# Kernel tuning notes

Measured on AMD Instinct MI355X. Metric: run time of the kernel, lower is better.

The kernel has to match this reference:

```python
import jax, jax.numpy as jnp
import numpy as np

B, L, DH = 4, 4096, 1024
T, DG = 1024, 768
P = 256


def setup_inputs() -> dict:
    key = jax.random.key(0)
    k1, k2, k3, k4, k5 = jax.random.split(key, 5)
    H = jax.random.normal(k1, (B, L, DH), dtype=jnp.float32)
    G = jax.random.normal(k2, (B, T, DG), dtype=jnp.float32)
    # key mask: True = padded/masked. Guarantee at least one valid key per row.
    mask = jax.random.randint(k3, (B, L), 0, 2).astype(jnp.bool_)
    mask = mask.at[:, 0].set(False)
    # torch Linear weights: [out, in]
    Wk_w = jax.random.normal(k4, (P, DH), dtype=jnp.float32) * (DH ** -0.5)
    Wq_w = jax.random.normal(k5, (P, DG), dtype=jnp.float32) * (DG ** -0.5)
    return {"H": H, "G": G, "mask": mask, "Wk_w": Wk_w, "Wq_w": Wq_w}


def reference(H, G, mask, Wk_w, Wq_w):
    # K = Wk(H): [B,L,P]; Q = Wq(G): [B,T,P]
    K = jnp.einsum('bld,pd->blp', H, Wk_w)
    Q = jnp.einsum('btd,pd->btp', G, Wq_w)
    scale = P ** -0.5
    logits = jnp.einsum('btp,blp->btl', Q, K) * scale  # [B,T,L]
    neg_inf = jnp.finfo(logits.dtype).min
    logits = jnp.where(mask[:, None, :], neg_inf, logits)
    alpha = jax.nn.softmax(logits, axis=-1)  # softmax over L (streaming-equivalent)
    Z = jnp.einsum('btl,bld->btd', alpha, H)  # [B,T,DH]
    return Z
```

## Files before the change

kernel.cpp:

```cpp
#include <hip/hip_runtime.h>
#include <hip/hip_bf16.h>


typedef __attribute__((ext_vector_type(8))) short short8;
typedef __attribute__((ext_vector_type(4))) float f32x4;

static __device__ __forceinline__ unsigned short bf16bits(float x) {
    __hip_bfloat16 b = __float2bfloat16(x);
    return *(unsigned short*)&b;
}

static __device__ __forceinline__ void gload_lds16(const __hip_bfloat16* g,
                                                   __hip_bfloat16* l)
{
    auto gp = (const __attribute__((address_space(1))) unsigned int*)(uintptr_t)g;
    auto lp = (__attribute__((address_space(3))) unsigned int*)(unsigned int)(uintptr_t)l;
    __builtin_amdgcn_global_load_lds(gp, lp, 16, 0, 0);
}

__global__ __launch_bounds__(256)
void scan_kernel(const void* __restrict__ mask,
                 unsigned short* __restrict__ idx,
                 int* __restrict__ lc, int* __restrict__ lcpad,
                 float* __restrict__ rowsum, int L, int T, int B)
{
    const int b = blockIdx.x;
    const int tid = threadIdx.x;

    for (int i = tid; i < T; i += 256) rowsum[(long)b * T + i] = 0.f;

    const unsigned char*  m8g  = (const unsigned char*)mask;
    const unsigned short* m16g = (const unsigned short*)mask;
    const unsigned int*   m32g = (const unsigned int*)mask;
    __shared__ int c1, c2, c4, c8, cp, wsh;
    if (tid == 0) { c1 = c2 = c4 = c8 = cp = 0; }
    __syncthreads();
    {
        const int N = B * L;
        int l1 = 0, l2 = 0, l4 = 0, l8 = 0, lp = 0;
        for (int i = tid; i < N; i += 256) l1 += (m8g[i] != 0);
        for (int i = tid; i < N / 2; i += 256) {
            l2 += (m16g[i] != 0);
            lp += ((m8g[2 * i] != 0) == (m8g[2 * i + 1] != 0));
        }
        for (int i = tid; i < N / 4; i += 256) l4 += (m32g[i] != 0);
        for (int i = tid; i < N / 8; i += 256) l8 += ((m32g[2 * i] | m32g[2 * i + 1]) != 0);
        atomicAdd(&c1, l1); atomicAdd(&c2, l2); atomicAdd(&c4, l4);
        atomicAdd(&c8, l8); atomicAdd(&cp, lp);
    }
    __syncthreads();
    if (tid == 0) {
        const float f1 = fabsf(c1 / 16384.f - 0.5f);
        const float f2 = fabsf(c2 / 8192.f  - 0.5f);
        const float f4 = fabsf(c4 / 4096.f  - 0.5f);
        const float f8 = fabsf(c8 / 2048.f  - 0.5f);
        int w = 1; float best = f1;
        if (f2 < best) { best = f2; w = 2; }
        if (f4 < best) { best = f4; w = 4; }
        if (f8 < best) { best = f8; w = 8; }
        if (w == 1 && cp > 7400) w = 2;
        wsh = w;
    }
    __syncthreads();
    const int w = wsh;

    const unsigned char*  m8  = (const unsigned char*)mask;
    const unsigned short* m16 = (const unsigned short*)mask;
    const unsigned int*   m32 = (const unsigned int*)mask;
    const uint2*          m64 = (const uint2*)mask;
    bool v[16];
    int cnt = 0;
    #pragma unroll
    for (int i = 0; i < 16; ++i) {
        const int l = tid * 16 + i;
        const long mi = (long)b * L + l;
        bool masked;
        if (w == 1)      masked = m8[mi] != 0;
        else if (w == 2) masked = m16[mi] != 0;
        else if (w == 4) masked = m32[mi] != 0;
        else             { uint2 q = m64[mi]; masked = (q.x | q.y) != 0; }
        v[i] = !masked;
        cnt += v[i] ? 1 : 0;
    }
    __shared__ int waveTot[4];
    int pre = cnt;
    #pragma unroll
    for (int off = 1; off < 64; off <<= 1) {
        const int t = __shfl_up(pre, off, 64);
        if ((tid & 63) >= off) pre += t;
    }
    if ((tid & 63) == 63) waveTot[tid >> 6] = pre;
    __syncthreads();
    int waveOff = 0;
    for (int wv = 0; wv < (tid >> 6); ++wv) waveOff += waveTot[wv];
    int o = waveOff + pre - cnt;
    #pragma unroll
    for (int i = 0; i < 16; ++i)
        if (v[i]) idx[(long)b * L + (o++)] = (unsigned short)(tid * 16 + i);
    if (tid == 255) {
        const int total = waveOff + pre;
        lc[b] = total;
        lcpad[b] = (total + 127) & ~127;
    }
}

__global__ __launch_bounds__(256)
void prep_all_kernel(const float* __restrict__ H,
                     __hip_bfloat16* __restrict__ Hbf,
                     __hip_bfloat16* __restrict__ Ht,
                     const unsigned short* __restrict__ idx,
                     const int* __restrict__ lc, const int* __restrict__ lcpad,
                     const float* __restrict__ Wk, unsigned short* __restrict__ Wkbf,
                     const float* __restrict__ Wq, unsigned short* __restrict__ Wqbf,
                     const float* __restrict__ G,  unsigned short* __restrict__ Gbf,
                     int L, int D)
{
    __shared__ __align__(16) __hip_bfloat16 tile[64][72];
    int id = blockIdx.x;
    if (id < 4096) {
        const int b  = id >> 10;
        const int c0 = (id & 63) * 64;
        if (c0 >= lcpad[b]) return;
        const int d0 = ((id >> 6) & 15) * 64;
        const int Lcb = lc[b];
        const float* Hb = H + (long)b * L * D;
        __hip_bfloat16* Hbfb = Hbf + (long)b * L * D;
        __hip_bfloat16* Htb  = Ht  + (long)b * D * L;
        const int tx = threadIdx.x & 15, ty = threadIdx.x >> 4;
        #pragma unroll
        for (int p = 0; p < 4; ++p) {
            const int row = ty + p * 16;
            const int c = c0 + row;
            float4 v = {0.f, 0.f, 0.f, 0.f};
            if (c < Lcb) {
                const int l = idx[(long)b * L + c];
                v = *(const float4*)(&Hb[(long)l * D + d0 + tx * 4]);
            }
            ushort4 o;
            o.x = bf16bits(v.x); o.y = bf16bits(v.y);
            o.z = bf16bits(v.z); o.w = bf16bits(v.w);
            *(ushort4*)(&Hbfb[(long)c * D + d0 + tx * 4]) = o;
            tile[tx * 4 + 0][row] = __float2bfloat16(v.x);
            tile[tx * 4 + 1][row] = __float2bfloat16(v.y);
            tile[tx * 4 + 2][row] = __float2bfloat16(v.z);
            tile[tx * 4 + 3][row] = __float2bfloat16(v.w);
        }
        __syncthreads();
        const int ll = threadIdx.x & 7;
        const int dq = threadIdx.x >> 3;
        #pragma unroll
        for (int q = 0; q < 2; ++q) {
            const int dd = dq + q * 32;
            const short8 v = *(const short8*)(&tile[dd][ll * 8]);
            *(short8*)(&Htb[(long)(d0 + dd) * L + c0 + ll * 8]) = v;
        }
        return;
    }
    id -= 4096;
    const float* in; unsigned short* out; int n4;
    if (id < 256)       { in = Wk; out = Wkbf; n4 = (256 * 1024) / 4; }
    else if (id < 448)  { id -= 256; in = Wq; out = Wqbf; n4 = (256 * 768) / 4; }
    else                { id -= 448; in = G;  out = Gbf;  n4 = (4 * 1024 * 768) / 4; }
    const int i = id * 256 + threadIdx.x;
    if (i >= n4) return;
    float4 v = ((const float4*)in)[i];
    ushort4 o;
    o.x = bf16bits(v.x); o.y = bf16bits(v.y);
    o.z = bf16bits(v.z); o.w = bf16bits(v.w);
    ((ushort4*)out)[i] = o;
}

template <typename OutT, int SPLITK, int MODE, int CMODE>
static __device__ __forceinline__
void gemm_bt_body(int bx, int by, int bz, __hip_bfloat16* lds_pool,
                  const __hip_bfloat16* __restrict__ A,
                  const __hip_bfloat16* __restrict__ Bm,
                  OutT* __restrict__ C,
                  int K, int lda, int ldb, int ldc,
                  long batchStrideA, long batchStrideB, long batchStrideC,
                  float scale,
                  float* __restrict__ rowsum, int rowsumStride,
                  long partStride,
                  const int* __restrict__ lc, const int* __restrict__ lcpad,
                  int Lfull)
{
    const int zb = bz / SPLITK;
    const int kc = bz % SPLITK;
    const int rowBase = bx * 128;
    const int colBase = by * 128;

    if constexpr (CMODE == 1) {
        const int bb = rowBase / Lfull;
        if (rowBase - bb * Lfull >= lcpad[bb]) return;
    }
    if constexpr (CMODE == 2) {
        if (colBase >= lcpad[zb]) return;
    }

    A  += (long)zb * batchStrideA;
    Bm += (long)zb * batchStrideB;
    C  += (long)zb * batchStrideC + (long)kc * partStride;
    int Kdyn = K;
    if constexpr (CMODE == 3) Kdyn = lcpad[zb];
    const int Kloc  = Kdyn / SPLITK;
    const int kbase = kc * Kloc;
    const int NT    = Kloc / 32;

    const int tid  = threadIdx.x;
    const int lane = tid & 63;
    const int wave = tid >> 6;
    const int wm = (wave & 1) * 64;
    const int wn = (wave >> 1) * 64;

    __hip_bfloat16* AsP = lds_pool;
    __hip_bfloat16* BsP = lds_pool + 12288;

    f32x4 acc[4][4];
    #pragma unroll
    for (int i = 0; i < 4; ++i)
        #pragma unroll
        for (int j = 0; j < 4; ++j)
            acc[i][j] = (f32x4){0.f, 0.f, 0.f, 0.f};

    const int srow = lane >> 2;
    const int scol = ((lane & 3) ^ ((lane >> 3) & 3)) * 8;
    const long ar0 = (long)(rowBase + wave * 32 + srow) * lda;
    const long ar1 = ar0 + 16l * lda;
    const long br0 = (long)(colBase + wave * 32 + srow) * ldb;
    const long br1 = br0 + 16l * ldb;

    const int mrow = lane & 15;
    const int koff = (((lane >> 4) ^ ((lane >> 1) & 3)) * 8);

    auto stage = [&](int buf, int t) {
        const int kk = kbase + t * 32 + scol;
        gload_lds16(A  + ar0 + kk, AsP + buf * 4096 + wave * 1024);
        gload_lds16(A  + ar1 + kk, AsP + buf * 4096 + wave * 1024 + 512);
        gload_lds16(Bm + br0 + kk, BsP + buf * 4096 + wave * 1024);
        gload_lds16(Bm + br1 + kk, BsP + buf * 4096 + wave * 1024 + 512);
    };

    stage(0, 0);
    if (NT > 1) stage(1, 1);

    int cur = 0;
    for (int t = 0; t < NT; ++t) {
        if (t + 1 < NT)
            asm volatile("s_waitcnt vmcnt(4)" ::: "memory");
        else
            asm volatile("s_waitcnt vmcnt(0)" ::: "memory");
        __builtin_amdgcn_s_barrier();
        if (t + 2 < NT) {
            const int nxt2 = (cur >= 1) ? cur - 1 : cur + 2;
            stage(nxt2, t + 2);
        }

        short8 af[4], bf[4];
        #pragma unroll
        for (int mi = 0; mi < 4; ++mi)
            af[mi] = *(const short8*)(AsP + cur * 4096 + (wm + mi * 16 + mrow) * 32 + koff);
        #pragma unroll
        for (int ni = 0; ni < 4; ++ni)
            bf[ni] = *(const short8*)(BsP + cur * 4096 + (wn + ni * 16 + mrow) * 32 + koff);

        #pragma unroll
        for (int mi = 0; mi < 4; ++mi)
            #pragma unroll
            for (int ni = 0; ni < 4; ++ni)
                acc[mi][ni] = __builtin_amdgcn_mfma_f32_16x16x32_bf16(
                    af[mi], bf[ni], acc[mi][ni], 0, 0, 0);
        cur = (cur == 2) ? 0 : cur + 1;
    }

    const int crow0 = (lane >> 4) * 4;
    const int ccol  = lane & 15;

    if constexpr (MODE == 2 || sizeof(OutT) == 2) {
        __syncthreads();
        __hip_bfloat16* cst = lds_pool;

        if constexpr (MODE == 2) {
            const int lcv = lc[zb];
            bool mk[4];
            #pragma unroll
            for (int ni = 0; ni < 4; ++ni)
                mk[ni] = (colBase + wn + ni * 16 + ccol) >= lcv;
            #pragma unroll
            for (int mi = 0; mi < 4; ++mi) {
                #pragma unroll
                for (int r = 0; r < 4; ++r) {
                    const int row = wm + mi * 16 + crow0 + r;
                    float rs = 0.f;
                    #pragma unroll
                    for (int ni = 0; ni < 4; ++ni) {
                        const int col = wn + ni * 16 + ccol;
                        const float e = mk[ni] ? 0.f
                                               : __expf(acc[mi][ni][r] * scale);
                        const __hip_bfloat16 pb = __float2bfloat16(e);
                        cst[row * 136 + (((col >> 3) ^ (row >> 3)) << 3) + (col & 7)] = pb;
                        rs += __bfloat162float(pb);
                    }
                    rs += __shfl_xor(rs, 1, 64);
                    rs += __shfl_xor(rs, 2, 64);
                    rs += __shfl_xor(rs, 4, 64);
                    rs += __shfl_xor(rs, 8, 64);
                    if ((lane & 15) == 0)
                        atomicAdd(&rowsum[(long)zb * rowsumStride + rowBase + row], rs);
                }
            }
        } else {
            #pragma unroll
            for (int mi = 0; mi < 4; ++mi) {
                #pragma unroll
                for (int ni = 0; ni < 4; ++ni) {
                    #pragma unroll
                    for (int r = 0; r < 4; ++r) {
                        const int row = wm + mi * 16 + crow0 + r;
                        const int col = wn + ni * 16 + ccol;
                        cst[row * 136 + (((col >> 3) ^ (row >> 3)) << 3) + (col & 7)] =
                            __float2bfloat16(acc[mi][ni][r] * scale);
                    }
                }
            }
        }
        __syncthreads();
        const int g   = tid & 15;
        const int r4  = tid >> 4;
        const int lof = ((g ^ r4) << 3);
        #pragma unroll
        for (int k = 0; k < 8; ++k) {
            const int row = r4 * 8 + k;
            const short8 v = *(const short8*)(cst + row * 136 + lof);
            *(short8*)(&((__hip_bfloat16*)C)[(long)(rowBase + row) * ldc + colBase + g * 8]) = v;
        }
    } else {
        #pragma unroll
        for (int mi = 0; mi < 4; ++mi) {
            #pragma unroll
            for (int ni = 0; ni < 4; ++ni) {
                #pragma unroll
                for (int r = 0; r < 4; ++r) {
                    const int row = rowBase + wm + mi * 16 + crow0 + r;
                    const int col = colBase + wn + ni * 16 + ccol;
                    ((float*)C)[(long)row * ldc + col] = acc[mi][ni][r] * scale;
                }
            }
        }
    }
}

static __device__ __forceinline__ void xcd_swizzle(int& bx, int& by, int& bz)
{
    const int nwg = gridDim.x * gridDim.y * gridDim.z;
    bx = blockIdx.x; by = blockIdx.y; bz = blockIdx.z;
    if ((nwg & 7) == 0) {
        int lin = bx + gridDim.x * (by + gridDim.y * bz);
        lin = (lin & 7) * (nwg >> 3) + (lin >> 3);
        bx = lin % gridDim.x;
        const int t = lin / gridDim.x;
        by = t % gridDim.y;
        bz = t / gridDim.y;
    }
}

template <typename OutT, int SPLITK, int MODE, int CMODE>
__global__ __launch_bounds__(256)
void gemm_bt_kernel(const __hip_bfloat16* __restrict__ A,
                    const __hip_bfloat16* __restrict__ Bm,
                    OutT* __restrict__ C,
                    int K, int lda, int ldb, int ldc,
                    long batchStrideA, long batchStrideB, long batchStrideC,
                    float scale,
                    float* __restrict__ rowsum, int rowsumStride,
                    long partStride,
                    const int* __restrict__ lc, const int* __restrict__ lcpad,
                    int Lfull)
{
    __shared__ __align__(16) __hip_bfloat16 lds_pool[24576];
    int bx, by, bz;
    xcd_swizzle(bx, by, bz);
    gemm_bt_body<OutT, SPLITK, MODE, CMODE>(bx, by, bz, lds_pool,
        A, Bm, C, K, lda, ldb, ldc, batchStrideA, batchStrideB, batchStrideC,
        scale, rowsum, rowsumStride, partStride, lc, lcpad, Lfull);
}

__global__ __launch_bounds__(256)
void qk_gemm_kernel(const __hip_bfloat16* __restrict__ Gbf,
                    const __hip_bfloat16* __restrict__ Wqbf,
                    __hip_bfloat16* __restrict__ Qbf,
                    const __hip_bfloat16* __restrict__ Hbf,
                    const __hip_bfloat16* __restrict__ Wkbf,
                    __hip_bfloat16* __restrict__ Kbf,
                    const int* __restrict__ lcpad,
                    int DG_, int DH_, int P_, int L_)
{
    __shared__ __align__(16) __hip_bfloat16 lds_pool[24576];
    int bx, by, bz;
    xcd_swizzle(bx, by, bz);
    if (bx < 32) {
        gemm_bt_body<__hip_bfloat16, 1, 0, 0>(bx, by, 0, lds_pool,
            Gbf, Wqbf, Qbf, DG_, DG_, DG_, P_, 0, 0, 0, 1.0f,
            nullptr, 0, 0, nullptr, nullptr, 0);
    } else {
        gemm_bt_body<__hip_bfloat16, 1, 0, 1>(bx - 32, by, 0, lds_pool,
            Hbf, Wkbf, Kbf, DH_, DH_, DH_, P_, 0, 0, 0, 1.0f,
            nullptr, 0, 0, nullptr, lcpad, L_);
    }
}

__global__ __launch_bounds__(256)
void combine_kernel(const float* __restrict__ Zp,
                    const float* __restrict__ rowsum,
                    float* __restrict__ Z, long partStride)
{
    const int i = blockIdx.x * 256 + threadIdx.x;
    const float4 a = ((const float4*)Zp)[i];
    const float4 b = ((const float4*)(Zp + partStride))[i];
    const float inv = 1.0f / rowsum[i >> 8];
    float4 o;
    o.x = (a.x + b.x) * inv;
    o.y = (a.y + b.y) * inv;
    o.z = (a.z + b.z) * inv;
    o.w = (a.w + b.w) * inv;
    ((float4*)Z)[i] = o;
}

extern "C" void kernel_launch(void* const* d_in, const int* in_sizes, int n_in,
                              void* d_out, int out_size, void* d_ws, size_t ws_size,
                              hipStream_t stream)
{
    constexpr int B = 4, L = 4096, DH = 1024, T = 1024, DG = 768, P = 256;

    const float* H  = (const float*)d_in[0];
    const float* G  = (const float*)d_in[1];
    const void*  mask = d_in[2];
    const float* Wk = (const float*)d_in[3];
    const float* Wq = (const float*)d_in[4];
    for (int i = 0; i < n_in; ++i) {
        switch (in_sizes[i]) {
            case B * L * DH: H    = (const float*)d_in[i]; break;
            case B * T * DG: G    = (const float*)d_in[i]; break;
            case B * L:      mask = d_in[i];               break;
            case P * DH:     Wk   = (const float*)d_in[i]; break;
            case P * DG:     Wq   = (const float*)d_in[i]; break;
        }
    }
    float* Z = (float*)d_out;

    char* ws = (char*)d_ws;
    __hip_bfloat16* Hbf  = (__hip_bfloat16*)ws;
    float*          Zp   = (float*)ws;
    __hip_bfloat16* Ht   = (__hip_bfloat16*)(ws + (32l << 20));
    __hip_bfloat16* Gbf  = (__hip_bfloat16*)(ws + (64l << 20));
    __hip_bfloat16* Qbf  = (__hip_bfloat16*)(ws + (70l << 20));
    __hip_bfloat16* Kbf  = (__hip_bfloat16*)(ws + (72l << 20));
    __hip_bfloat16* Wkbf = (__hip_bfloat16*)(ws + (80l << 20));
    __hip_bfloat16* Wqbf = (__hip_bfloat16*)(ws + (80l << 20) + (512l << 10));
    float*          rowsum    = (float*)(ws + (80l << 20) + (896l << 10));
    int*            lcBuf     = (int*)  (ws + (80l << 20) + (961l << 10));
    int*            lcpadBuf  = (int*)  (ws + (80l << 20) + (961l << 10) + 64);
    unsigned short* idxBuf    = (unsigned short*)(ws + (80l << 20) + (962l << 10));
    __hip_bfloat16* Sb   = (__hip_bfloat16*)(ws + (81l << 20));

    constexpr long ZPART = (long)B * T * DH;

    const dim3 blk(256);

    scan_kernel<<<dim3(B), blk, 0, stream>>>(
        mask, idxBuf, lcBuf, lcpadBuf, rowsum, L, T, B);

    prep_all_kernel<<<dim3(7616), blk, 0, stream>>>(
        H, Hbf, Ht, idxBuf, lcBuf, lcpadBuf,
        Wk, (unsigned short*)Wkbf, Wq, (unsigned short*)Wqbf,
        G, (unsigned short*)Gbf, L, DH);

    qk_gemm_kernel<<<dim3(160, 2, 1), blk, 0, stream>>>(
        Gbf, Wqbf, Qbf, Hbf, Wkbf, Kbf, lcpadBuf, DG, DH, P, L);

    gemm_bt_kernel<__hip_bfloat16, 1, 2, 2><<<dim3(T / 128, L / 128, B), blk, 0, stream>>>(
        Qbf, Kbf, Sb, P, P, P, L,
        (long)T * P, (long)L * P, (long)T * L, 0.0625f,
        rowsum, T, 0, lcBuf, lcpadBuf, L);
    gemm_bt_kernel<float, 2, 0, 3><<<dim3(T / 128, DH / 128, B * 2), blk, 0, stream>>>(
        Sb, Ht, Zp, L, L, L, DH,
        (long)T * L, (long)DH * L, (long)T * DH, 1.0f,
        nullptr, 0, ZPART, nullptr, lcpadBuf, L);
    combine_kernel<<<dim3((B * T * DH / 4) / 256), blk, 0, stream>>>(
        Zp, rowsum, Z, ZPART);
}
```

Baseline: 219.9 us.

## Replace split-K Z GEMM and combine pass with 64-row tiles and fused normalization

The alpha·H GEMM no longer uses split-K=2 with fp32 partials followed by a separate combine kernel. Instead it uses 64-row A tiles, which gives the same block count without splitting K, and divides by the row sum directly in the epilogue. This removes the partial-sum write/read traffic (two fp32 B×T×DH buffers) and one kernel launch. In exchange each block runs the full K loop and reuses less of each B tile per block, and the output stores are scalar fp32 writes.

```diff
diff --git a/kernel.cpp b/kernel.cpp
--- a/kernel.cpp
+++ b/kernel.cpp
@@ -170,61 +170,47 @@
     ((ushort4*)out)[i] = o;
 }
 
-template <typename OutT, int SPLITK, int MODE, int CMODE>
+template <typename OutT, int MODE, int BM>
 static __device__ __forceinline__
-void gemm_bt_body(int bx, int by, int bz, __hip_bfloat16* lds_pool,
+void gemm_bt_body(int bx, int by, int zb, __hip_bfloat16* lds_pool,
                   const __hip_bfloat16* __restrict__ A,
                   const __hip_bfloat16* __restrict__ Bm,
                   OutT* __restrict__ C,
                   int K, int lda, int ldb, int ldc,
                   long batchStrideA, long batchStrideB, long batchStrideC,
                   float scale,
-                  float* __restrict__ rowsum, int rowsumStride,
-                  long partStride,
-                  const int* __restrict__ lc, const int* __restrict__ lcpad,
-                  int Lfull)
-{
-    const int zb = bz / SPLITK;
-    const int kc = bz % SPLITK;
-    const int rowBase = bx * 128;
-    const int colBase = by * 128;
-
-    if constexpr (CMODE == 1) {
-        const int bb = rowBase / Lfull;
-        if (rowBase - bb * Lfull >= lcpad[bb]) return;
-    }
-    if constexpr (CMODE == 2) {
-        if (colBase >= lcpad[zb]) return;
-    }
+                  float* __restrict__ rowsum, int rowsumStride, int lcv)
+{
+    constexpr int MI  = BM / 32;
+    constexpr int ACH = BM / 64;
+    constexpr int ATS = BM * 32;
 
     A  += (long)zb * batchStrideA;
     Bm += (long)zb * batchStrideB;
-    C  += (long)zb * batchStrideC + (long)kc * partStride;
-    int Kdyn = K;
-    if constexpr (CMODE == 3) Kdyn = lcpad[zb];
-    const int Kloc  = Kdyn / SPLITK;
-    const int kbase = kc * Kloc;
-    const int NT    = Kloc / 32;
+    C  += (long)zb * batchStrideC;
+    const int NT = K / 32;
 
     const int tid  = threadIdx.x;
     const int lane = tid & 63;
     const int wave = tid >> 6;
-    const int wm = (wave & 1) * 64;
+    const int wm = (wave & 1) * (BM / 2);
     const int wn = (wave >> 1) * 64;
+    const int rowBase = bx * BM;
+    const int colBase = by * 128;
 
     __hip_bfloat16* AsP = lds_pool;
-    __hip_bfloat16* BsP = lds_pool + 12288;
-
-    f32x4 acc[4][4];
+    __hip_bfloat16* BsP = lds_pool + 3 * ATS;
+
+    f32x4 acc[MI][4];
     #pragma unroll
-    for (int i = 0; i < 4; ++i)
+    for (int i = 0; i < MI; ++i)
         #pragma unroll
         for (int j = 0; j < 4; ++j)
             acc[i][j] = (f32x4){0.f, 0.f, 0.f, 0.f};
 
     const int srow = lane >> 2;
     const int scol = ((lane & 3) ^ ((lane >> 3) & 3)) * 8;
-    const long ar0 = (long)(rowBase + wave * 32 + srow) * lda;
+    const long ar0 = (long)(rowBase + wave * (BM / 4) + srow) * lda;
     const long ar1 = ar0 + 16l * lda;
     const long br0 = (long)(colBase + wave * 32 + srow) * ldb;
     const long br1 = br0 + 16l * ldb;
@@ -233,38 +219,43 @@
     const int koff = (((lane >> 4) ^ ((lane >> 1) & 3)) * 8);
 
     auto stage = [&](int buf, int t) {
-        const int kk = kbase + t * 32 + scol;
-        gload_lds16(A  + ar0 + kk, AsP + buf * 4096 + wave * 1024);
-        gload_lds16(A  + ar1 + kk, AsP + buf * 4096 + wave * 1024 + 512);
+        const int kk = t * 32 + scol;
+        gload_lds16(A + ar0 + kk, AsP + buf * ATS + wave * (BM / 4) * 32);
+        if constexpr (ACH == 2)
+            gload_lds16(A + ar1 + kk, AsP + buf * ATS + wave * (BM / 4) * 32 + 512);
         gload_lds16(Bm + br0 + kk, BsP + buf * 4096 + wave * 1024);
         gload_lds16(Bm + br1 + kk, BsP + buf * 4096 + wave * 1024 + 512);
     };
 
     stage(0, 0);
-    if (NT > 1) stage(1, 1);
+    stage(1, 1);
 
     int cur = 0;
     for (int t = 0; t < NT; ++t) {
-        if (t + 1 < NT)
-            asm volatile("s_waitcnt vmcnt(4)" ::: "memory");
-        else
+        if (t + 1 < NT) {
+            if constexpr (ACH == 2)
+                asm volatile("s_waitcnt vmcnt(4)" ::: "memory");
+            else
+                asm volatile("s_waitcnt vmcnt(3)" ::: "memory");
+        } else {
             asm volatile("s_waitcnt vmcnt(0)" ::: "memory");
+        }
         __builtin_amdgcn_s_barrier();
         if (t + 2 < NT) {
             const int nxt2 = (cur >= 1) ? cur - 1 : cur + 2;
             stage(nxt2, t + 2);
         }
 
-        short8 af[4], bf[4];
-        #pragma unroll
-        for (int mi = 0; mi < 4; ++mi)
-            af[mi] = *(const short8*)(AsP + cur * 4096 + (wm + mi * 16 + mrow) * 32 + koff);
+        short8 af[MI], bf[4];
+        #pragma unroll
+        for (int mi = 0; mi < MI; ++mi)
+            af[mi] = *(const short8*)(AsP + cur * ATS + (wm + mi * 16 + mrow) * 32 + koff);
         #pragma unroll
         for (int ni = 0; ni < 4; ++ni)
             bf[ni] = *(const short8*)(BsP + cur * 4096 + (wn + ni * 16 + mrow) * 32 + koff);
 
         #pragma unroll
-        for (int mi = 0; mi < 4; ++mi)
+        for (int mi = 0; mi < MI; ++mi)
             #pragma unroll
             for (int ni = 0; ni < 4; ++ni)
                 acc[mi][ni] = __builtin_amdgcn_mfma_f32_16x16x32_bf16(
@@ -275,52 +266,34 @@
     const int crow0 = (lane >> 4) * 4;
     const int ccol  = lane & 15;
 
-    if constexpr (MODE == 2 || sizeof(OutT) == 2) {
+    if constexpr (MODE == 2) {
         __syncthreads();
         __hip_bfloat16* cst = lds_pool;
-
-        if constexpr (MODE == 2) {
-            const int lcv = lc[zb];
-            bool mk[4];
+        bool mk[4];
+        #pragma unroll
+        for (int ni = 0; ni < 4; ++ni)
+            mk[ni] = (colBase + wn + ni * 16 + ccol) >= lcv;
+        #pragma unroll
+        for (int mi = 0; mi < MI; ++mi) {
             #pragma unroll
-            for (int ni = 0; ni < 4; ++ni)
-                mk[ni] = (colBase + wn + ni * 16 + ccol) >= lcv;
-            #pragma unroll
-            for (int mi = 0; mi < 4; ++mi) {
-                #pragma unroll
-                for (int r = 0; r < 4; ++r) {
-                    const int row = wm + mi * 16 + crow0 + r;
-                    float rs = 0.f;
-                    #pragma unroll
-                    for (int ni = 0; ni < 4; ++ni) {
-                        const int col = wn + ni * 16 + ccol;
-                        const float e = mk[ni] ? 0.f
-                                               : __expf(acc[mi][ni][r] * scale);
-                        const __hip_bfloat16 pb = __float2bfloat16(e);
-                        cst[row * 136 + (((col >> 3) ^ (row >> 3)) << 3) + (col & 7)] = pb;
-                        rs += __bfloat162float(pb);
-                    }
-                    rs += __shfl_xor(rs, 1, 64);
-                    rs += __shfl_xor(rs, 2, 64);
-                    rs += __shfl_xor(rs, 4, 64);
-                    rs += __shfl_xor(rs, 8, 64);
-                    if ((lane & 15) == 0)
-                        atomicAdd(&rowsum[(long)zb * rowsumStride + rowBase + row], rs);
-                }
-            }
-        } else {
-            #pragma unroll
-            for (int mi = 0; mi < 4; ++mi) {
+            for (int r = 0; r < 4; ++r) {
+                const int row = wm + mi * 16 + crow0 + r;
+                float rs = 0.f;
                 #pragma unroll
                 for (int ni = 0; ni < 4; ++ni) {
-                    #pragma unroll
-                    for (int r = 0; r < 4; ++r) {
-                        const int row = wm + mi * 16 + crow0 + r;
-                        const int col = wn + ni * 16 + ccol;
-                        cst[row * 136 + (((col >> 3) ^ (row >> 3)) << 3) + (col & 7)] =
-                            __float2bfloat16(acc[mi][ni][r] * scale);
-                    }
+                    const int col = wn + ni * 16 + ccol;
+                    const float e = mk[ni] ? 0.f
+                                           : __expf(acc[mi][ni][r] * scale);
+                    const __hip_bfloat16 pb = __float2bfloat16(e);
+                    cst[row * 136 + (((col >> 3) ^ (row >> 3)) << 3) + (col & 7)] = pb;
+                    rs += __bfloat162float(pb);
                 }
+                rs += __shfl_xor(rs, 1, 64);
+                rs += __shfl_xor(rs, 2, 64);
+                rs += __shfl_xor(rs, 4, 64);
+                rs += __shfl_xor(rs, 8, 64);
+                if ((lane & 15) == 0)
+                    atomicAdd(&rowsum[(long)zb * rowsumStride + rowBase + row], rs);
             }
         }
         __syncthreads();
@@ -333,9 +306,49 @@
             const short8 v = *(const short8*)(cst + row * 136 + lof);
             *(short8*)(&((__hip_bfloat16*)C)[(long)(rowBase + row) * ldc + colBase + g * 8]) = v;
         }
+    } else if constexpr (MODE == 3) {
+        #pragma unroll
+        for (int mi = 0; mi < MI; ++mi) {
+            #pragma unroll
+            for (int r = 0; r < 4; ++r) {
+                const int row = rowBase + wm + mi * 16 + crow0 + r;
+                const float inv = 1.0f / rowsum[(long)zb * rowsumStride + row];
+                #pragma unroll
+                for (int ni = 0; ni < 4; ++ni) {
+                    const int col = colBase + wn + ni * 16 + ccol;
+                    ((float*)C)[(long)row * ldc + col] = acc[mi][ni][r] * inv;
+                }
+            }
+        }
+    } else if constexpr (sizeof(OutT) == 2) {
+        __syncthreads();
+        __hip_bfloat16* cst = lds_pool;
+        #pragma unroll
+        for (int mi = 0; mi < MI; ++mi) {
+            #pragma unroll
+            for (int ni = 0; ni < 4; ++ni) {
+                #pragma unroll
+                for (int r = 0; r < 4; ++r) {
+                    const int row = wm + mi * 16 + crow0 + r;
+                    const int col = wn + ni * 16 + ccol;
+                    cst[row * 136 + (((col >> 3) ^ (row >> 3)) << 3) + (col & 7)] =
+                        __float2bfloat16(acc[mi][ni][r] * scale);
+                }
+            }
+        }
+        __syncthreads();
+        const int g   = tid & 15;
+        const int r4  = tid >> 4;
+        const int lof = ((g ^ r4) << 3);
+        #pragma unroll
+        for (int k = 0; k < 8; ++k) {
+            const int row = r4 * 8 + k;
+            const short8 v = *(const short8*)(cst + row * 136 + lof);
+            *(short8*)(&((__hip_bfloat16*)C)[(long)(rowBase + row) * ldc + colBase + g * 8]) = v;
+        }
     } else {
         #pragma unroll
-        for (int mi = 0; mi < 4; ++mi) {
+        for (int mi = 0; mi < MI; ++mi) {
             #pragma unroll
             for (int ni = 0; ni < 4; ++ni) {
                 #pragma unroll
@@ -363,27 +376,6 @@
     }
 }
 
-template <typename OutT, int SPLITK, int MODE, int CMODE>
-__global__ __launch_bounds__(256)
-void gemm_bt_kernel(const __hip_bfloat16* __restrict__ A,
-                    const __hip_bfloat16* __restrict__ Bm,
-                    OutT* __restrict__ C,
-                    int K, int lda, int ldb, int ldc,
-                    long batchStrideA, long batchStrideB, long batchStrideC,
-                    float scale,
-                    float* __restrict__ rowsum, int rowsumStride,
-                    long partStride,
-                    const int* __restrict__ lc, const int* __restrict__ lcpad,
-                    int Lfull)
-{
-    __shared__ __align__(16) __hip_bfloat16 lds_pool[24576];
-    int bx, by, bz;
-    xcd_swizzle(bx, by, bz);
-    gemm_bt_body<OutT, SPLITK, MODE, CMODE>(bx, by, bz, lds_pool,
-        A, Bm, C, K, lda, ldb, ldc, batchStrideA, batchStrideB, batchStrideC,
-        scale, rowsum, rowsumStride, partStride, lc, lcpad, Lfull);
-}
-
 __global__ __launch_bounds__(256)
 void qk_gemm_kernel(const __hip_bfloat16* __restrict__ Gbf,
                     const __hip_bfloat16* __restrict__ Wqbf,
@@ -398,31 +390,52 @@
     int bx, by, bz;
     xcd_swizzle(bx, by, bz);
     if (bx < 32) {
-        gemm_bt_body<__hip_bfloat16, 1, 0, 0>(bx, by, 0, lds_pool,
+        gemm_bt_body<__hip_bfloat16, 0, 128>(bx, by, 0, lds_pool,
             Gbf, Wqbf, Qbf, DG_, DG_, DG_, P_, 0, 0, 0, 1.0f,
-            nullptr, 0, 0, nullptr, nullptr, 0);
+            nullptr, 0, 0);
     } else {
-        gemm_bt_body<__hip_bfloat16, 1, 0, 1>(bx - 32, by, 0, lds_pool,
+        const int rowBase = (bx - 32) * 128;
+        const int bb = rowBase / L_;
+        if (rowBase - bb * L_ >= lcpad[bb]) return;
+        gemm_bt_body<__hip_bfloat16, 0, 128>(bx - 32, by, 0, lds_pool,
             Hbf, Wkbf, Kbf, DH_, DH_, DH_, P_, 0, 0, 0, 1.0f,
-            nullptr, 0, 0, nullptr, lcpad, L_);
+            nullptr, 0, 0);
     }
 }
 
 __global__ __launch_bounds__(256)
-void combine_kernel(const float* __restrict__ Zp,
-                    const float* __restrict__ rowsum,
-                    float* __restrict__ Z, long partStride)
-{
-    const int i = blockIdx.x * 256 + threadIdx.x;
-    const float4 a = ((const float4*)Zp)[i];
-    const float4 b = ((const float4*)(Zp + partStride))[i];
-    const float inv = 1.0f / rowsum[i >> 8];
-    float4 o;
-    o.x = (a.x + b.x) * inv;
-    o.y = (a.y + b.y) * inv;
-    o.z = (a.z + b.z) * inv;
-    o.w = (a.w + b.w) * inv;
-    ((float4*)Z)[i] = o;
+void s_gemm_kernel(const __hip_bfloat16* __restrict__ Qbf,
+                   const __hip_bfloat16* __restrict__ Kbf,
+                   __hip_bfloat16* __restrict__ Sb,
+                   const int* __restrict__ lc, const int* __restrict__ lcpad,
+                   float* __restrict__ rowsum,
+                   int P_, int L_, int T_)
+{
+    __shared__ __align__(16) __hip_bfloat16 lds_pool[24576];
+    int bx, by, bz;
+    xcd_swizzle(bx, by, bz);
+    if (by * 128 >= lcpad[bz]) return;
+    gemm_bt_body<__hip_bfloat16, 2, 128>(bx, by, bz, lds_pool,
+        Qbf, Kbf, Sb, P_, P_, P_, L_,
+        (long)T_ * P_, (long)L_ * P_, (long)T_ * L_, 0.0625f,
+        rowsum, T_, lc[bz]);
+}
+
+__global__ __launch_bounds__(256)
+void z_gemm_kernel(const __hip_bfloat16* __restrict__ Sb,
+                   const __hip_bfloat16* __restrict__ Ht,
+                   float* __restrict__ Z,
+                   const int* __restrict__ lcpad,
+                   const float* __restrict__ rowsum,
+                   int L_, int DH_, int T_)
+{
+    __shared__ __align__(16) __hip_bfloat16 lds_pool[24576];
+    int bx, by, bz;
+    xcd_swizzle(bx, by, bz);
+    gemm_bt_body<float, 3, 64>(bx, by, bz, lds_pool,
+        Sb, Ht, Z, lcpad[bz], L_, L_, DH_,
+        (long)T_ * L_, (long)DH_ * L_, (long)T_ * DH_, 1.0f,
+        (float*)rowsum, T_, 0);
 }
 
 extern "C" void kernel_launch(void* const* d_in, const int* in_sizes, int n_in,
@@ -449,7 +462,6 @@
 
     char* ws = (char*)d_ws;
     __hip_bfloat16* Hbf  = (__hip_bfloat16*)ws;
-    float*          Zp   = (float*)ws;
     __hip_bfloat16* Ht   = (__hip_bfloat16*)(ws + (32l << 20));
     __hip_bfloat16* Gbf  = (__hip_bfloat16*)(ws + (64l << 20));
     __hip_bfloat16* Qbf  = (__hip_bfloat16*)(ws + (70l << 20));
@@ -462,8 +474,6 @@
     unsigned short* idxBuf    = (unsigned short*)(ws + (80l << 20) + (962l << 10));
     __hip_bfloat16* Sb   = (__hip_bfloat16*)(ws + (81l << 20));
 
-    constexpr long ZPART = (long)B * T * DH;
-
     const dim3 blk(256);
 
     scan_kernel<<<dim3(B), blk, 0, stream>>>(
@@ -477,14 +487,9 @@
     qk_gemm_kernel<<<dim3(160, 2, 1), blk, 0, stream>>>(
         Gbf, Wqbf, Qbf, Hbf, Wkbf, Kbf, lcpadBuf, DG, DH, P, L);
 
-    gemm_bt_kernel<__hip_bfloat16, 1, 2, 2><<<dim3(T / 128, L / 128, B), blk, 0, stream>>>(
-        Qbf, Kbf, Sb, P, P, P, L,
-        (long)T * P, (long)L * P, (long)T * L, 0.0625f,
-        rowsum, T, 0, lcBuf, lcpadBuf, L);
-    gemm_bt_kernel<float, 2, 0, 3><<<dim3(T / 128, DH / 128, B * 2), blk, 0, stream>>>(
-        Sb, Ht, Zp, L, L, L, DH,
-        (long)T * L, (long)DH * L, (long)T * DH, 1.0f,
-        nullptr, 0, ZPART, nullptr, lcpadBuf, L);
-    combine_kernel<<<dim3((B * T * DH / 4) / 256), blk, 0, stream>>>(
-        Zp, rowsum, Z, ZPART);
-}
+    s_gemm_kernel<<<dim3(T / 128, L / 128, B), blk, 0, stream>>>(
+        Qbf, Kbf, Sb, lcBuf, lcpadBuf, rowsum, P, L, T);
+
+    z_gemm_kernel<<<dim3(T / 64, DH / 128, B), blk, 0, stream>>>(
+        Sb, Ht, Z, lcpadBuf, rowsum, L, DH, T);
+}
```

Measured after the change: 217.2 us. Within noise of the previous version (-1.2%).
